# Kernel optimization log

Hardware: AMD Instinct MI355X
Metric: run time of the kernel (lower is better)

The kernel has to match this reference:

```python
import jax, jax.numpy as jnp
import numpy as np

EPS = 1e-5


def _gn(v, axes, gamma, beta):
    # GroupNorm: normalize over `axes` per (batch, group), then affine.
    mu = jnp.mean(v, axis=axes, keepdims=True)
    var = jnp.var(v, axis=axes, keepdims=True)
    return (v - mu) * jax.lax.rsqrt(var + EPS) * gamma + beta


def setup_inputs() -> dict:
    key = jax.random.key(0)
    ks = jax.random.split(key, 5)
    B, G, BW, S, CD, H = 8, 32, 64, 64, 256, 64
    x = jax.random.normal(ks[0], (B, G * BW, H, H), jnp.float32)
    sent_embs = jax.random.normal(ks[1], (B, CD), jnp.float32)
    # grouped 1x1 conv weights stored as [group, out_per_group, in_per_group]
    Wq = jax.random.normal(ks[2], (G, S, CD), jnp.float32) * 0.05
    Wk = jax.random.normal(ks[3], (G, S, BW), jnp.float32) * 0.05
    Wv = jax.random.normal(ks[4], (G, S, BW), jnp.float32) * 0.05
    gamma1 = jnp.ones((G * S,), jnp.float32)
    beta1 = jnp.zeros((G * S,), jnp.float32)
    gamma2 = jnp.ones((G * S,), jnp.float32)
    beta2 = jnp.zeros((G * S,), jnp.float32)
    return {"x": x, "sent_embs": sent_embs, "Wq": Wq, "Wk": Wk, "Wv": Wv,
            "gamma1": gamma1, "beta1": beta1, "gamma2": gamma2, "beta2": beta2}


def reference(x, sent_embs, Wq, Wk, Wv, gamma1, beta1, gamma2, beta2):
    G, S, CD = Wq.shape
    B, C, H, W = x.shape
    BW = C // G
    xr = x.reshape(B, G, BW, H * W)                    # [B,G,bw,N]
    # query: same sent_emb broadcast to every group, grouped 1x1 conv
    q = jnp.einsum('bc,gsc->bgs', sent_embs, Wq)       # [B,G,S]
    q = _gn(q, (2,), gamma1.reshape(G, S), beta1.reshape(G, S))
    # key: grouped 1x1 conv over spatial map
    k = jnp.einsum('bgcn,gsc->bgsn', xr, Wk)           # [B,G,S,N]
    k = _gn(k, (2, 3), gamma2.reshape(G, S, 1), beta2.reshape(G, S, 1))
    # single-query attention per (batch, group)
    sim = jnp.einsum('bgs,bgsn->bgn', q, k)            # [B,G,N]
    attn = jax.nn.softmax(sim, axis=-1)
    out = jnp.einsum('bgn,bgcn->bgc', attn, xr)        # [B,G,bw]
    out = jnp.einsum('bgc,gsc->bgs', out, Wv)          # value grouped conv
    return out.reshape(B, G * S, 1, 1)
```

## Files before the change

### kernel.cpp

```cpp
#include <hip/hip_runtime.h>
#include <stdint.h>


#define EPS 1e-5f
#define NN 4096
#define CHUNK 256
#define NCHUNK 16

typedef __bf16 bf16x8 __attribute__((ext_vector_type(8)));
typedef float f32x4 __attribute__((ext_vector_type(4)));
typedef short short8 __attribute__((ext_vector_type(8)));

__device__ __forceinline__ unsigned short f2bf(float f) {
  unsigned u = __builtin_bit_cast(unsigned, f);
  u += 0x7fffu + ((u >> 16) & 1u);
  return (unsigned short)(u >> 16);
}

__global__ __launch_bounds__(64) void kA(const float* __restrict__ sent,
                                         const float* __restrict__ Wq,
                                         const float* __restrict__ Wk,
                                         const float* __restrict__ g1,
                                         const float* __restrict__ b1,
                                         const float* __restrict__ g2,
                                         float* __restrict__ w_all,
                                         float* __restrict__ sums,
                                         float* __restrict__ outc) {
  int bg = blockIdx.x; int b = bg >> 5; int g = bg & 31;
  int t = threadIdx.x;
  const float* wqrow = Wq + (size_t)(g * 64 + t) * 256;
  const float* se = sent + b * 256;
  float q = 0.f;
  for (int c = 0; c < 256; c += 4) {
    float4 wv = *(const float4*)(wqrow + c);
    q += se[c] * wv.x + se[c + 1] * wv.y + se[c + 2] * wv.z + se[c + 3] * wv.w;
  }
  float s = q;
  for (int off = 32; off; off >>= 1) s += __shfl_xor(s, off);
  float mu = s * (1.f / 64.f);
  float d = q - mu;
  float v = d * d;
  for (int off = 32; off; off >>= 1) v += __shfl_xor(v, off);
  float rsq = rsqrtf(v * (1.f / 64.f) + EPS);
  int gs = g * 64 + t;
  float qh = d * rsq * g1[gs] + b1[gs];
  float qg2 = qh * g2[gs];
  __shared__ float qs[64];
  qs[t] = qg2;
  __syncthreads();
  float wacc = 0.f;
  for (int s2 = 0; s2 < 64; s2++)
    wacc += qs[s2] * Wk[(size_t)(g * 64 + s2) * 64 + t];
  w_all[bg * 64 + t] = wacc;
  outc[bg * 64 + t] = 0.f;
  if (t < 2) sums[bg * 2 + t] = 0.f;
}

__global__ __launch_bounds__(256, 4) void kB(const float* __restrict__ x,
                                             const float* __restrict__ Wk,
                                             const float* __restrict__ w_all,
                                             float* __restrict__ y_all,
                                             float* __restrict__ sums) {
  int bg = blockIdx.y; int b = bg >> 5; int g = bg & 31;
  int n0 = blockIdx.x * CHUNK;
  int t = threadIdx.x;
  int lane = t & 63;
  int wv = t >> 6;

  __shared__ unsigned short xt[64 * 260];
  __shared__ float ypart[4 * 256];
  __shared__ float red[8];

  bf16x8 afr[4][2];
  {
    int sA = lane & 15, khi = lane >> 4;
    for (int st = 0; st < 4; st++)
      for (int cc = 0; cc < 2; cc++) {
        short8 tmp;
        const float* wkrow = Wk + (size_t)(g * 64 + st * 16 + sA) * 64 + cc * 32 + khi * 8;
        #pragma unroll
        for (int j = 0; j < 8; j++) tmp[j] = (short)f2bf(wkrow[j]);
        afr[st][cc] = __builtin_bit_cast(bf16x8, tmp);
      }
  }

  const float* xb = x + ((size_t)(b * 2048 + g * 64)) * NN + n0;
  const float* wp = w_all + bg * 64;
  float y0 = 0, y1 = 0, y2 = 0, y3 = 0;
  #pragma unroll 4
  for (int k = 0; k < 16; k++) {
    int c = wv + 4 * k;
    float4 vx = *(const float4*)(xb + (size_t)c * NN + lane * 4);
    float wc = wp[c];
    y0 += wc * vx.x; y1 += wc * vx.y; y2 += wc * vx.z; y3 += wc * vx.w;
    unsigned p0 = ((unsigned)f2bf(vx.y) << 16) | f2bf(vx.x);
    unsigned p1 = ((unsigned)f2bf(vx.w) << 16) | f2bf(vx.z);
    uint2 pk; pk.x = p0; pk.y = p1;
    *(uint2*)&xt[c * 260 + lane * 4] = pk;
  }
  {
    float4 yp; yp.x = y0; yp.y = y1; yp.z = y2; yp.w = y3;
    *(float4*)&ypart[wv * 256 + lane * 4] = yp;
  }
  __syncthreads();
  y_all[(size_t)bg * NN + n0 + t] =
      ypart[t] + ypart[256 + t] + ypart[512 + t] + ypart[768 + t];

  float sk1 = 0.f, sk2 = 0.f;
  int nB = lane & 15;
  int kB_ = (lane >> 4) * 8;
  #pragma unroll
  for (int nt = 0; nt < 4; nt++) {
    int nb = wv * 64 + nt * 16 + nB;
    short8 b0t, b1t;
    #pragma unroll
    for (int j = 0; j < 8; j++) {
      b0t[j] = (short)xt[(kB_ + j) * 260 + nb];
      b1t[j] = (short)xt[(32 + kB_ + j) * 260 + nb];
    }
    bf16x8 bf0 = __builtin_bit_cast(bf16x8, b0t);
    bf16x8 bf1 = __builtin_bit_cast(bf16x8, b1t);
    #pragma unroll
    for (int st = 0; st < 4; st++) {
      f32x4 acc = {0.f, 0.f, 0.f, 0.f};
      acc = __builtin_amdgcn_mfma_f32_16x16x32_bf16(afr[st][0], bf0, acc, 0, 0, 0);
      acc = __builtin_amdgcn_mfma_f32_16x16x32_bf16(afr[st][1], bf1, acc, 0, 0, 0);
      sk1 += acc[0] + acc[1] + acc[2] + acc[3];
      sk2 += acc[0] * acc[0] + acc[1] * acc[1] + acc[2] * acc[2] + acc[3] * acc[3];
    }
  }
  for (int off = 32; off; off >>= 1) {
    sk1 += __shfl_xor(sk1, off);
    sk2 += __shfl_xor(sk2, off);
  }
  if (lane == 0) { red[wv] = sk1; red[4 + wv] = sk2; }
  __syncthreads();
  if (t == 0) {
    atomicAdd(&sums[bg * 2 + 0], red[0] + red[1] + red[2] + red[3]);
    atomicAdd(&sums[bg * 2 + 1], red[4] + red[5] + red[6] + red[7]);
  }
}

__global__ __launch_bounds__(256) void kC(const float* __restrict__ y_all,
                                          const float* __restrict__ sums,
                                          float* __restrict__ attn) {
  int bg = blockIdx.x; int t = threadIdx.x;
  float s1 = sums[bg * 2], s2 = sums[bg * 2 + 1];
  float mu = s1 * (1.f / 262144.f);
  float var = s2 * (1.f / 262144.f) - mu * mu;
  float rs = rsqrtf(var + EPS);
  const float* y = y_all + (size_t)bg * NN;
  float l[16];
  float m = -1e30f;
  #pragma unroll
  for (int i = 0; i < 16; i++) {
    l[i] = rs * y[t + 256 * i];
    m = fmaxf(m, l[i]);
  }
  __shared__ float red[8];
  for (int off = 32; off; off >>= 1) m = fmaxf(m, __shfl_xor(m, off));
  int wv = t >> 6, lane = t & 63;
  if (lane == 0) red[wv] = m;
  __syncthreads();
  m = fmaxf(fmaxf(red[0], red[1]), fmaxf(red[2], red[3]));
  float sum = 0.f;
  #pragma unroll
  for (int i = 0; i < 16; i++) { l[i] = __expf(l[i] - m); sum += l[i]; }
  for (int off = 32; off; off >>= 1) sum += __shfl_xor(sum, off);
  if (lane == 0) red[4 + wv] = sum;
  __syncthreads();
  float inv = 1.f / (red[4] + red[5] + red[6] + red[7]);
  float* ao = attn + (size_t)bg * NN;
  #pragma unroll
  for (int i = 0; i < 16; i++) ao[t + 256 * i] = l[i] * inv;
}

__global__ __launch_bounds__(256) void kD(const float* __restrict__ x,
                                          const float* __restrict__ attn,
                                          float* __restrict__ outc) {
  int bg = 255 - blockIdx.y; int b = bg >> 5; int g = bg & 31;
  int n0 = (NCHUNK - 1 - blockIdx.x) * CHUNK;
  int t = threadIdx.x; int lane = t & 63; int wv = t >> 6;
  const float* xb = x + ((size_t)(b * 2048 + g * 64)) * NN + n0;
  float4 a = *(const float4*)(attn + (size_t)bg * NN + n0 + lane * 4);
  float p[16];
  #pragma unroll 4
  for (int k = 0; k < 16; k++) {
    int c = wv + 4 * k;
    float4 vx = *(const float4*)(xb + (size_t)c * NN + lane * 4);
    p[k] = a.x * vx.x + a.y * vx.y + a.z * vx.z + a.w * vx.w;
  }
  #pragma unroll
  for (int k = 0; k < 16; k++) {
    float r = p[k];
    for (int off = 32; off; off >>= 1) r += __shfl_xor(r, off);
    if (lane == 0) atomicAdd(&outc[bg * 64 + wv + 4 * k], r);
  }
}

__global__ __launch_bounds__(64) void kE(const float* __restrict__ outc,
                                         const float* __restrict__ Wv,
                                         float* __restrict__ out) {
  int bg = blockIdx.x; int g = bg & 31;
  int t = threadIdx.x;
  __shared__ float oc[64];
  __shared__ float wvs[64 * 65];
  oc[t] = outc[bg * 64 + t];
  const float* wg = Wv + (size_t)g * 4096;
  for (int i = 0; i < 64; i++) wvs[i * 65 + t] = wg[i * 64 + t];
  __syncthreads();
  float acc = 0.f;
  for (int c = 0; c < 64; c++) acc += wvs[t * 65 + c] * oc[c];
  out[bg * 64 + t] = acc;
}

extern "C" void kernel_launch(void* const* d_in, const int* in_sizes, int n_in,
                              void* d_out, int out_size, void* d_ws, size_t ws_size,
                              hipStream_t stream) {
  const float* x    = (const float*)d_in[0];
  const float* sent = (const float*)d_in[1];
  const float* Wq   = (const float*)d_in[2];
  const float* Wk   = (const float*)d_in[3];
  const float* Wv   = (const float*)d_in[4];
  const float* g1   = (const float*)d_in[5];
  const float* b1   = (const float*)d_in[6];
  const float* g2   = (const float*)d_in[7];
  float* out = (float*)d_out;

  char* ws = (char*)d_ws;
  float* w_all = (float*)(ws);
  float* sums  = (float*)(ws + 65536);
  float* outc  = (float*)(ws + 67584);
  float* y_all = (float*)(ws + 133120);
  float* attn  = (float*)(ws + 133120 + 4194304);

  kA<<<256, 64, 0, stream>>>(sent, Wq, Wk, g1, b1, g2, w_all, sums, outc);
  kB<<<dim3(NCHUNK, 256), 256, 0, stream>>>(x, Wk, w_all, y_all, sums);
  kC<<<256, 256, 0, stream>>>(y_all, sums, attn);
  kD<<<dim3(NCHUNK, 256), 256, 0, stream>>>(x, attn, outc);
  kE<<<256, 64, 0, stream>>>(outc, Wv, out);
}
```

Before: 429.1 us.

## Compute GroupNorm stats via Gram matrix and replace atomics with partial buffers

The key-variance computation is reformulated. Instead of forming k = Wk·x with MFMA and squaring it, each block builds the x Gram matrix X·Xᵀ with MFMA and contracts it against a precomputed M = WkᵀWk (new kM kernel). The mean comes from column sums of Wk. Atomics in kB and kD are replaced by per-chunk partial buffers that kC and kE reduce, which also removes the zero-init from kA. kD is coarsened to process four chunks per block. The bf16 rounding becomes a cheaper round-half-up, and the LDS stride changes to 264. This adds an extra launch and a small amount of M loading per block.

```diff
diff --git a/kernel.cpp b/kernel.cpp
--- a/kernel.cpp
+++ b/kernel.cpp
@@ -6,16 +6,10 @@
 #define NN 4096
 #define CHUNK 256
 #define NCHUNK 16
+#define NSTR 264
 
 typedef __bf16 bf16x8 __attribute__((ext_vector_type(8)));
 typedef float f32x4 __attribute__((ext_vector_type(4)));
-typedef short short8 __attribute__((ext_vector_type(8)));
-
-__device__ __forceinline__ unsigned short f2bf(float f) {
-  unsigned u = __builtin_bit_cast(unsigned, f);
-  u += 0x7fffu + ((u >> 16) & 1u);
-  return (unsigned short)(u >> 16);
-}
 
 __global__ __launch_bounds__(64) void kA(const float* __restrict__ sent,
                                          const float* __restrict__ Wq,
@@ -23,9 +17,7 @@
                                          const float* __restrict__ g1,
                                          const float* __restrict__ b1,
                                          const float* __restrict__ g2,
-                                         float* __restrict__ w_all,
-                                         float* __restrict__ sums,
-                                         float* __restrict__ outc) {
+                                         float* __restrict__ w_all) {
   int bg = blockIdx.x; int b = bg >> 5; int g = bg & 31;
   int t = threadIdx.x;
   const float* wqrow = Wq + (size_t)(g * 64 + t) * 256;
@@ -43,8 +35,7 @@
   for (int off = 32; off; off >>= 1) v += __shfl_xor(v, off);
   float rsq = rsqrtf(v * (1.f / 64.f) + EPS);
   int gs = g * 64 + t;
-  float qh = d * rsq * g1[gs] + b1[gs];
-  float qg2 = qh * g2[gs];
+  float qg2 = (d * rsq * g1[gs] + b1[gs]) * g2[gs];
   __shared__ float qs[64];
   qs[t] = qg2;
   __syncthreads();
@@ -52,51 +43,72 @@
   for (int s2 = 0; s2 < 64; s2++)
     wacc += qs[s2] * Wk[(size_t)(g * 64 + s2) * 64 + t];
   w_all[bg * 64 + t] = wacc;
-  outc[bg * 64 + t] = 0.f;
-  if (t < 2) sums[bg * 2 + t] = 0.f;
+}
+
+__global__ __launch_bounds__(256) void kM(const float* __restrict__ Wk,
+                                          float* __restrict__ M,
+                                          float* __restrict__ cw) {
+  int g = blockIdx.x; int t = threadIdx.x;
+  __shared__ float wk[4096];
+  const float* wg = Wk + (size_t)g * 4096;
+  #pragma unroll
+  for (int i = 0; i < 16; i++) wk[t + 256 * i] = wg[t + 256 * i];
+  __syncthreads();
+  int c = t & 63, q = t >> 6;
+  float acc[16];
+  #pragma unroll
+  for (int i = 0; i < 16; i++) acc[i] = 0.f;
+  for (int s = 0; s < 64; s++) {
+    float a = wk[s * 64 + c];
+    const float* r = &wk[s * 64 + q * 16];
+    #pragma unroll
+    for (int i = 0; i < 16; i++) acc[i] += a * r[i];
+  }
+  float* Mg = M + (size_t)g * 4096;
+  #pragma unroll
+  for (int i = 0; i < 16; i++) Mg[(q * 16 + i) * 64 + c] = acc[i];
+  if (t < 64) {
+    float s2 = 0.f;
+    for (int s = 0; s < 64; s++) s2 += wk[s * 64 + t];
+    cw[g * 64 + t] = s2;
+  }
 }
 
 __global__ __launch_bounds__(256, 4) void kB(const float* __restrict__ x,
-                                             const float* __restrict__ Wk,
                                              const float* __restrict__ w_all,
+                                             const float* __restrict__ cw,
+                                             const float* __restrict__ M,
                                              float* __restrict__ y_all,
-                                             float* __restrict__ sums) {
+                                             float* __restrict__ sums_part) {
   int bg = blockIdx.y; int b = bg >> 5; int g = bg & 31;
   int n0 = blockIdx.x * CHUNK;
   int t = threadIdx.x;
   int lane = t & 63;
   int wv = t >> 6;
 
-  __shared__ unsigned short xt[64 * 260];
+  __shared__ unsigned short xt[64 * NSTR];
   __shared__ float ypart[4 * 256];
   __shared__ float red[8];
 
-  bf16x8 afr[4][2];
-  {
-    int sA = lane & 15, khi = lane >> 4;
-    for (int st = 0; st < 4; st++)
-      for (int cc = 0; cc < 2; cc++) {
-        short8 tmp;
-        const float* wkrow = Wk + (size_t)(g * 64 + st * 16 + sA) * 64 + cc * 32 + khi * 8;
-        #pragma unroll
-        for (int j = 0; j < 8; j++) tmp[j] = (short)f2bf(wkrow[j]);
-        afr[st][cc] = __builtin_bit_cast(bf16x8, tmp);
-      }
-  }
-
   const float* xb = x + ((size_t)(b * 2048 + g * 64)) * NN + n0;
   const float* wp = w_all + bg * 64;
-  float y0 = 0, y1 = 0, y2 = 0, y3 = 0;
+  const float* cwp = cw + g * 64;
+  float y0 = 0, y1 = 0, y2 = 0, y3 = 0, zt = 0;
   #pragma unroll 4
   for (int k = 0; k < 16; k++) {
     int c = wv + 4 * k;
     float4 vx = *(const float4*)(xb + (size_t)c * NN + lane * 4);
-    float wc = wp[c];
+    float wc = wp[c], cc = cwp[c];
     y0 += wc * vx.x; y1 += wc * vx.y; y2 += wc * vx.z; y3 += wc * vx.w;
-    unsigned p0 = ((unsigned)f2bf(vx.y) << 16) | f2bf(vx.x);
-    unsigned p1 = ((unsigned)f2bf(vx.w) << 16) | f2bf(vx.z);
-    uint2 pk; pk.x = p0; pk.y = p1;
-    *(uint2*)&xt[c * 260 + lane * 4] = pk;
+    zt += cc * (vx.x + vx.y + vx.z + vx.w);
+    unsigned a0 = __builtin_bit_cast(unsigned, vx.x) + 0x8000u;
+    unsigned a1 = __builtin_bit_cast(unsigned, vx.y) + 0x8000u;
+    unsigned a2 = __builtin_bit_cast(unsigned, vx.z) + 0x8000u;
+    unsigned a3 = __builtin_bit_cast(unsigned, vx.w) + 0x8000u;
+    uint2 pk;
+    pk.x = (a0 >> 16) | (a1 & 0xffff0000u);
+    pk.y = (a2 >> 16) | (a3 & 0xffff0000u);
+    *(uint2*)&xt[c * NSTR + lane * 4] = pk;
   }
   {
     float4 yp; yp.x = y0; yp.y = y1; yp.z = y2; yp.w = y3;
@@ -106,46 +118,55 @@
   y_all[(size_t)bg * NN + n0 + t] =
       ypart[t] + ypart[256 + t] + ypart[512 + t] + ypart[768 + t];
 
-  float sk1 = 0.f, sk2 = 0.f;
-  int nB = lane & 15;
-  int kB_ = (lane >> 4) * 8;
-  #pragma unroll
-  for (int nt = 0; nt < 4; nt++) {
-    int nb = wv * 64 + nt * 16 + nB;
-    short8 b0t, b1t;
-    #pragma unroll
-    for (int j = 0; j < 8; j++) {
-      b0t[j] = (short)xt[(kB_ + j) * 260 + nb];
-      b1t[j] = (short)xt[(32 + kB_ + j) * 260 + nb];
+  int rbase = (lane & 15) * NSTR;
+  int koff = (lane >> 4) * 8;
+  f32x4 acc[4];
+  #pragma unroll
+  for (int r = 0; r < 4; r++) acc[r] = (f32x4){0.f, 0.f, 0.f, 0.f};
+  #pragma unroll
+  for (int kk = 0; kk < 8; kk++) {
+    bf16x8 frg[4];
+    #pragma unroll
+    for (int r = 0; r < 4; r++)
+      frg[r] = *(const bf16x8*)&xt[r * 16 * NSTR + rbase + kk * 32 + koff];
+    bf16x8 af = frg[wv];
+    #pragma unroll
+    for (int r = 0; r < 4; r++)
+      acc[r] = __builtin_amdgcn_mfma_f32_16x16x32_bf16(af, frg[r], acc[r], 0, 0, 0);
+  }
+  float s2acc = 0.f;
+  {
+    const float* Mg = M + (size_t)g * 4096;
+    int row = wv * 16 + (lane >> 4) * 4, col = lane & 15;
+    #pragma unroll
+    for (int r = 0; r < 4; r++) {
+      const float* mrow = Mg + r * 16 + col;
+      #pragma unroll
+      for (int i = 0; i < 4; i++) s2acc += acc[r][i] * mrow[(row + i) * 64];
     }
-    bf16x8 bf0 = __builtin_bit_cast(bf16x8, b0t);
-    bf16x8 bf1 = __builtin_bit_cast(bf16x8, b1t);
-    #pragma unroll
-    for (int st = 0; st < 4; st++) {
-      f32x4 acc = {0.f, 0.f, 0.f, 0.f};
-      acc = __builtin_amdgcn_mfma_f32_16x16x32_bf16(afr[st][0], bf0, acc, 0, 0, 0);
-      acc = __builtin_amdgcn_mfma_f32_16x16x32_bf16(afr[st][1], bf1, acc, 0, 0, 0);
-      sk1 += acc[0] + acc[1] + acc[2] + acc[3];
-      sk2 += acc[0] * acc[0] + acc[1] * acc[1] + acc[2] * acc[2] + acc[3] * acc[3];
-    }
   }
   for (int off = 32; off; off >>= 1) {
-    sk1 += __shfl_xor(sk1, off);
-    sk2 += __shfl_xor(sk2, off);
-  }
-  if (lane == 0) { red[wv] = sk1; red[4 + wv] = sk2; }
+    zt += __shfl_xor(zt, off);
+    s2acc += __shfl_xor(s2acc, off);
+  }
+  if (lane == 0) { red[wv] = zt; red[4 + wv] = s2acc; }
   __syncthreads();
   if (t == 0) {
-    atomicAdd(&sums[bg * 2 + 0], red[0] + red[1] + red[2] + red[3]);
-    atomicAdd(&sums[bg * 2 + 1], red[4] + red[5] + red[6] + red[7]);
+    float* sp = sums_part + (size_t)(blockIdx.x * 256 + bg) * 2;
+    sp[0] = red[0] + red[1] + red[2] + red[3];
+    sp[1] = red[4] + red[5] + red[6] + red[7];
   }
 }
 
 __global__ __launch_bounds__(256) void kC(const float* __restrict__ y_all,
-                                          const float* __restrict__ sums,
+                                          const float* __restrict__ sums_part,
                                           float* __restrict__ attn) {
   int bg = blockIdx.x; int t = threadIdx.x;
-  float s1 = sums[bg * 2], s2 = sums[bg * 2 + 1];
+  float s1 = 0.f, s2 = 0.f;
+  for (int i = 0; i < NCHUNK; i++) {
+    const float* sp = sums_part + (size_t)(i * 256 + bg) * 2;
+    s1 += sp[0]; s2 += sp[1];
+  }
   float mu = s1 * (1.f / 262144.f);
   float var = s2 * (1.f / 262144.f) - mu * mu;
   float rs = rsqrtf(var + EPS);
@@ -175,37 +196,44 @@
   for (int i = 0; i < 16; i++) ao[t + 256 * i] = l[i] * inv;
 }
 
-__global__ __launch_bounds__(256) void kD(const float* __restrict__ x,
-                                          const float* __restrict__ attn,
-                                          float* __restrict__ outc) {
+__global__ __launch_bounds__(256, 4) void kD(const float* __restrict__ x,
+                                             const float* __restrict__ attn,
+                                             float* __restrict__ outp) {
   int bg = 255 - blockIdx.y; int b = bg >> 5; int g = bg & 31;
-  int n0 = (NCHUNK - 1 - blockIdx.x) * CHUNK;
+  int n0b = (3 - blockIdx.x) * 1024;
   int t = threadIdx.x; int lane = t & 63; int wv = t >> 6;
-  const float* xb = x + ((size_t)(b * 2048 + g * 64)) * NN + n0;
-  float4 a = *(const float4*)(attn + (size_t)bg * NN + n0 + lane * 4);
+  const float* xb = x + ((size_t)(b * 2048 + g * 64)) * NN;
+  const float* ab = attn + (size_t)bg * NN;
   float p[16];
-  #pragma unroll 4
-  for (int k = 0; k < 16; k++) {
-    int c = wv + 4 * k;
-    float4 vx = *(const float4*)(xb + (size_t)c * NN + lane * 4);
-    p[k] = a.x * vx.x + a.y * vx.y + a.z * vx.z + a.w * vx.w;
+  #pragma unroll
+  for (int k = 0; k < 16; k++) p[k] = 0.f;
+  for (int s = 0; s < 4; s++) {
+    int n0 = n0b + s * 256;
+    float4 a = *(const float4*)(ab + n0 + lane * 4);
+    #pragma unroll 4
+    for (int k = 0; k < 16; k++) {
+      int c = wv + 4 * k;
+      float4 vx = *(const float4*)(xb + (size_t)c * NN + n0 + lane * 4);
+      p[k] += a.x * vx.x + a.y * vx.y + a.z * vx.z + a.w * vx.w;
+    }
   }
   #pragma unroll
   for (int k = 0; k < 16; k++) {
     float r = p[k];
     for (int off = 32; off; off >>= 1) r += __shfl_xor(r, off);
-    if (lane == 0) atomicAdd(&outc[bg * 64 + wv + 4 * k], r);
-  }
-}
-
-__global__ __launch_bounds__(64) void kE(const float* __restrict__ outc,
+    if (lane == 0) outp[(size_t)blockIdx.x * 16384 + bg * 64 + wv + 4 * k] = r;
+  }
+}
+
+__global__ __launch_bounds__(64) void kE(const float* __restrict__ outp,
                                          const float* __restrict__ Wv,
                                          float* __restrict__ out) {
   int bg = blockIdx.x; int g = bg & 31;
   int t = threadIdx.x;
   __shared__ float oc[64];
   __shared__ float wvs[64 * 65];
-  oc[t] = outc[bg * 64 + t];
+  oc[t] = outp[bg * 64 + t] + outp[16384 + bg * 64 + t] +
+          outp[32768 + bg * 64 + t] + outp[49152 + bg * 64 + t];
   const float* wg = Wv + (size_t)g * 4096;
   for (int i = 0; i < 64; i++) wvs[i * 65 + t] = wg[i * 64 + t];
   __syncthreads();
@@ -229,14 +257,17 @@
 
   char* ws = (char*)d_ws;
   float* w_all = (float*)(ws);
-  float* sums  = (float*)(ws + 65536);
-  float* outc  = (float*)(ws + 67584);
-  float* y_all = (float*)(ws + 133120);
-  float* attn  = (float*)(ws + 133120 + 4194304);
-
-  kA<<<256, 64, 0, stream>>>(sent, Wq, Wk, g1, b1, g2, w_all, sums, outc);
-  kB<<<dim3(NCHUNK, 256), 256, 0, stream>>>(x, Wk, w_all, y_all, sums);
-  kC<<<256, 256, 0, stream>>>(y_all, sums, attn);
-  kD<<<dim3(NCHUNK, 256), 256, 0, stream>>>(x, attn, outc);
-  kE<<<256, 64, 0, stream>>>(outc, Wv, out);
-}
+  float* cw    = (float*)(ws + 65536);
+  float* M     = (float*)(ws + 73728);
+  float* sumsp = (float*)(ws + 598016);
+  float* outp  = (float*)(ws + 630784);
+  float* y_all = (float*)(ws + 892928);
+  float* attn  = (float*)(ws + 5087232);
+
+  kA<<<256, 64, 0, stream>>>(sent, Wq, Wk, g1, b1, g2, w_all);
+  kM<<<32, 256, 0, stream>>>(Wk, M, cw);
+  kB<<<dim3(NCHUNK, 256), 256, 0, stream>>>(x, w_all, cw, M, y_all, sumsp);
+  kC<<<256, 256, 0, stream>>>(y_all, sumsp, attn);
+  kD<<<dim3(4, 256), 256, 0, stream>>>(x, attn, outp);
+  kE<<<256, 64, 0, stream>>>(outp, Wv, out);
+}
```

Result: slower. 529.5 us (+23.4%).
